# Kernel optimization log

Hardware: AMD Instinct MI355X
Metric: run time of the kernel (lower is better)

## Reference

```python
import jax, jax.numpy as jnp
import numpy as np

N, IN_CH, HID, OUT = 3072, 128, 256, 32
HEADS = 12


def setup_inputs() -> dict:
    key = jax.random.key(0)
    ks = jax.random.split(key, 16)

    def glorot(k, shape):
        fan_in, fan_out = shape[0], shape[-1]
        lim = float(np.sqrt(6.0 / (fan_in + fan_out)))
        return jax.random.uniform(k, shape, jnp.float32, -lim, lim)

    return {
        "x": jax.random.normal(ks[0], (N, IN_CH), jnp.float32),
        "attn_tensor": jax.random.normal(ks[1], (HEADS, N, N), jnp.float32),
        "edge_weight": jnp.ones((1,), jnp.float32),  # unused (use_edge_weight=False)
        "batch_idx": jnp.zeros((N,), jnp.int64),      # single graph
        # Conv2d(12,1,1) == per-head scalar mix
        "agg_w": jax.random.normal(ks[2], (HEADS,), jnp.float32) * 0.1,
        "agg_b": jnp.zeros((1,), jnp.float32),
        # GCNConv weights (x @ W then propagate, + bias)
        "W1": glorot(ks[3], (IN_CH, HID)), "b1": jnp.zeros((HID,), jnp.float32),
        "W2": glorot(ks[4], (HID, HID)),   "b2": jnp.zeros((HID,), jnp.float32),
        # final MLP: Linear -> ReLU -> LayerNorm -> Linear
        "lin1_W": glorot(ks[5], (HID, HID)), "lin1_b": jnp.zeros((HID,), jnp.float32),
        "ln_g": jnp.ones((HID,), jnp.float32), "ln_b": jnp.zeros((HID,), jnp.float32),
        "lin2_W": glorot(ks[6], (HID, OUT)), "lin2_b": jnp.zeros((OUT,), jnp.float32),
    }


def reference(x, attn_tensor, edge_weight, batch_idx,
              agg_w, agg_b, W1, b1, W2, b2,
              lin1_W, lin1_b, ln_g, ln_b, lin2_W, lin2_b):
    threshold = 0.0
    n = x.shape[0]

    # Conv2d(12,1,kernel_size=1): weighted sum over heads -> [N, N] score matrix
    agg = jnp.einsum('c,cij->ij', agg_w, attn_tensor) + agg_b[0]

    # thresholded adjacency (mask.nonzero() -> edge_index), kept dense in jax
    A = (agg > threshold).astype(x.dtype)  # A[s, t] = edge s->t

    # PyG gcn_norm with add_remaining_self_loops (binary weights -> diag = 1)
    eye = jnp.eye(n, dtype=x.dtype)
    A_hat = A * (1.0 - eye) + eye
    deg = A_hat.sum(axis=0)                        # in-degree at target nodes
    dinv = jnp.where(deg > 0, jax.lax.rsqrt(deg), 0.0)
    A_norm = dinv[:, None] * A_hat * dinv[None, :]  # norm = dinv[src] * dinv[dst]

    # GCNConv 1: out[t] = sum_s A_norm[s,t] (x W)[s] + b
    h = jnp.einsum('st,sd->td', A_norm, x @ W1) + b1
    h = jax.nn.relu(h)
    # GCNConv 2
    h = jnp.einsum('st,sd->td', A_norm, h @ W2) + b2

    # global_mean_pool over batch_idx (single graph here)
    bi = batch_idx.astype(jnp.int32)
    sums = jax.ops.segment_sum(h, bi, num_segments=1)
    counts = jax.ops.segment_sum(jnp.ones((n,), h.dtype), bi, num_segments=1)
    g = sums / counts[:, None]

    # Linear -> ReLU -> LayerNorm -> Linear
    z = jax.nn.relu(g @ lin1_W + lin1_b)
    mu = z.mean(axis=-1, keepdims=True)
    var = ((z - mu) ** 2).mean(axis=-1, keepdims=True)
    z = (z - mu) * jax.lax.rsqrt(var + 1e-5) * ln_g + ln_b
    out = z @ lin2_W + lin2_b
    return out
```

## Files before the change

### kernel.cpp

```cpp
#include <hip/hip_runtime.h>
#include <hip/hip_bf16.h>

#define NN     3072
#define NW32   96
#define INCH   128
#define HID    256
#define NHEADS 12
#define PLANE  9437184LL
#define NADJ   2304
#define CHUNK  4096

typedef __attribute__((ext_vector_type(8))) short     s16x8;
typedef __attribute__((ext_vector_type(4))) float     f32x4;
typedef __attribute__((ext_vector_type(8))) unsigned short u16x8;
typedef __attribute__((ext_vector_type(4))) unsigned int   u32x4;

__device__ inline unsigned short bf16_rne(float f) {
    unsigned int u = __float_as_uint(f);
    u += 0x7FFFu + ((u >> 16) & 1u);
    return (unsigned short)(u >> 16);
}

__global__ __launch_bounds__(256) void k_adj_y1(const float* __restrict__ attn,
                                                const float* __restrict__ agg_w,
                                                const float* __restrict__ agg_b,
                                                const float* __restrict__ x,
                                                const float* __restrict__ W1,
                                                unsigned int* __restrict__ mask32,
                                                unsigned short* __restrict__ y1t) {
    __shared__ unsigned char nib[1024];
    __shared__ float xs[8][INCH];

    if (blockIdx.x < NADJ) {
        const int b = blockIdx.x;
        const int j = threadIdx.x;
        const float thr = -agg_b[0];
        float wc[NHEADS];
#pragma unroll
        for (int c = 0; c < NHEADS; ++c) wc[c] = agg_w[c];

        f32x4 acc[4];
#pragma unroll
        for (int sl = 0; sl < 4; ++sl) acc[sl] = (f32x4){0.f, 0.f, 0.f, 0.f};

        const float* pb = attn + (long long)b * CHUNK + 4 * j;
#pragma unroll 1
        for (int c = 0; c < NHEADS; ++c) {
            const float* pc = pb + (long long)c * PLANE;
            const float w = wc[c];
            f32x4 v0 = *(const f32x4*)(pc);
            f32x4 v1 = *(const f32x4*)(pc + 1024);
            f32x4 v2 = *(const f32x4*)(pc + 2048);
            f32x4 v3 = *(const f32x4*)(pc + 3072);
#pragma unroll
            for (int k = 0; k < 4; ++k) {
                acc[0][k] = fmaf(w, v0[k], acc[0][k]);
                acc[1][k] = fmaf(w, v1[k], acc[1][k]);
                acc[2][k] = fmaf(w, v2[k], acc[2][k]);
                acc[3][k] = fmaf(w, v3[k], acc[3][k]);
            }
        }

        const unsigned B = (unsigned)b * CHUNK;
#pragma unroll
        for (int sl = 0; sl < 4; ++sl) {
            const unsigned i0 = B + sl * 1024u + 4u * j;
            unsigned bits = 0;
#pragma unroll
            for (int k = 0; k < 4; ++k) {
                bool pred = (acc[sl][k] > thr) || ((i0 + k) % 3073u == 0u);
                bits |= pred ? (1u << k) : 0u;
            }
            nib[sl * 256 + j] = (unsigned char)bits;
        }
        __syncthreads();
        if (j < 128) {
            unsigned a  = *(const unsigned*)(nib + 8 * j);
            unsigned c2 = *(const unsigned*)(nib + 8 * j + 4);
            a  &= 0x0F0F0F0Fu; a  = (a  | (a  >> 4)) & 0x00FF00FFu; a  = (a  | (a  >> 8)) & 0x0000FFFFu;
            c2 &= 0x0F0F0F0Fu; c2 = (c2 | (c2 >> 4)) & 0x00FF00FFu; c2 = (c2 | (c2 >> 8)) & 0x0000FFFFu;
            mask32[(B >> 5) + j] = a | (c2 << 16);
        }
    } else {
        int s0 = (blockIdx.x - NADJ) * 8;
        for (int i = threadIdx.x; i < 8 * INCH; i += 256)
            xs[i >> 7][i & 127] = x[s0 * INCH + i];
        __syncthreads();
        int d = threadIdx.x;
        float acc[8] = {0, 0, 0, 0, 0, 0, 0, 0};
        for (int k = 0; k < INCH; ++k) {
            float w = W1[k * HID + d];
#pragma unroll
            for (int r = 0; r < 8; ++r) acc[r] = fmaf(xs[r][k], w, acc[r]);
        }
        u16x8 v;
#pragma unroll
        for (int r = 0; r < 8; ++r) v[r] = bf16_rne(acc[r]);
        *(u16x8*)(y1t + (long long)d * NN + s0) = v;
    }
}

__global__ __launch_bounds__(256) void k_pack(const unsigned int* __restrict__ mask32,
                                              unsigned long long* __restrict__ maskT64) {
    const int w = threadIdx.x >> 6, l = threadIdx.x & 63;
    const int tile = blockIdx.x * 4 + w;
    const int sq = tile % 48, tq = tile / 48;
    const unsigned long long* m64 = (const unsigned long long*)mask32;
    unsigned long long myw = m64[(long long)(sq * 64 + l) * 48 + tq];
#pragma unroll 8
    for (int tt = 0; tt < 64; ++tt) {
        unsigned long long bal = __ballot((myw >> tt) & 1ULL);
        if (l == tt)
            maskT64[(long long)(tq * 64 + tt) * 48 + sq] = bal;
    }
}

__global__ __launch_bounds__(256) void k_dinv(const unsigned int* __restrict__ maskT32,
                                              float* __restrict__ dinv,
                                              unsigned short* __restrict__ dinvb) {
    int t = blockIdx.x * 256 + threadIdx.x;
    const u32x4* row = (const u32x4*)(maskT32 + (long long)t * NW32);
    int deg = 0;
#pragma unroll
    for (int i = 0; i < 24; ++i) {
        u32x4 v = row[i];
        deg += __popc(v[0]) + __popc(v[1]) + __popc(v[2]) + __popc(v[3]);
    }
    float di = rsqrtf((float)deg);
    dinv[t] = di;
    dinvb[t] = bf16_rne(di);
}

__global__ __launch_bounds__(256) void k_prop(const unsigned int* __restrict__ maskT32,
                                              const unsigned short* __restrict__ dinvb,
                                              const unsigned short* __restrict__ y1t,
                                              const float* __restrict__ dinv,
                                              float* __restrict__ partials,
                                              float* __restrict__ w2p) {
    if (blockIdx.x < 384) {
        const int w = threadIdx.x >> 6, l = threadIdx.x & 63;
        const int lr = l & 15, lg = l >> 4;
        const int t0 = (blockIdx.x % 48) * 64 + w * 16;
        const int d0 = ((blockIdx.x / 48) % 2) * 128;
        const int z  = blockIdx.x / 96;

        const unsigned long long* mrow =
            (const unsigned long long*)(maskT32 + (long long)(t0 + lr) * NW32) + z * 12;

        const unsigned short* B[8];
#pragma unroll
        for (int n = 0; n < 8; ++n)
            B[n] = y1t + (long long)(d0 + n * 16 + lr) * NN;

        f32x4 acc[8];
#pragma unroll
        for (int n = 0; n < 8; ++n) acc[n] = (f32x4){0.f, 0.f, 0.f, 0.f};

#pragma unroll 2
        for (int kw = 0; kw < 12; ++kw) {
            unsigned long long word = mrow[kw];
#pragma unroll
            for (int half = 0; half < 2; ++half) {
                const int k0 = z * 768 + kw * 64 + half * 32 + lg * 8;
                unsigned int bits = (unsigned int)((word >> (half * 32 + lg * 8)) & 0xFFULL);
                u16x8 dv = *(const u16x8*)(dinvb + k0);
                s16x8 av;
#pragma unroll
                for (int j = 0; j < 8; ++j)
                    av[j] = ((bits >> j) & 1u) ? (short)dv[j] : (short)0;
#pragma unroll
                for (int n = 0; n < 8; ++n) {
                    s16x8 bv = *(const s16x8*)(const void*)(B[n] + k0);
                    acc[n] = __builtin_amdgcn_mfma_f32_16x16x32_bf16(av, bv, acc[n], 0, 0, 0);
                }
            }
        }

        const int trow = t0 + lg * 4;
#pragma unroll
        for (int n = 0; n < 8; ++n) {
            const int d = d0 + n * 16 + lr;
#pragma unroll
            for (int r = 0; r < 4; ++r)
                partials[((size_t)z * NN + trow + r) * HID + d] = acc[n][r];
        }
    } else {
        __shared__ float red[4][64];
        const int r = blockIdx.x - 384;
        const int wq = r % 48;
        const int tc = r / 48;
        const int wv = threadIdx.x >> 6, l = threadIdx.x & 63;
        const unsigned long long* mt = (const unsigned long long*)maskT32;
        float acc = 0.0f;
#pragma unroll 4
        for (int it = 0; it < 64; ++it) {
            const int t = tc * 256 + wv * 64 + it;
            unsigned long long word = mt[(long long)t * 48 + wq];
            acc += ((word >> l) & 1ULL) ? dinv[t] : 0.0f;
        }
        red[wv][l] = acc;
        __syncthreads();
        if (threadIdx.x < 64)
            w2p[tc * NN + wq * 64 + threadIdx.x] =
                red[0][threadIdx.x] + red[1][threadIdx.x] + red[2][threadIdx.x] + red[3][threadIdx.x];
    }
}

__global__ __launch_bounds__(256) void k_vred(const float* __restrict__ partials,
                                              const float* __restrict__ dinv,
                                              const float* __restrict__ b1,
                                              const float* __restrict__ w2p,
                                              float* __restrict__ vp) {
    __shared__ float w2s[8];
    const int b = blockIdx.x, d = threadIdx.x;
    if (threadIdx.x < 8) {
        const int t = b * 8 + threadIdx.x;
        float a = 0.0f;
#pragma unroll
        for (int tc = 0; tc < 12; ++tc) a += w2p[tc * NN + t];
        w2s[threadIdx.x] = dinv[t] * a;
    }
    __syncthreads();
    const float bb = b1[d];
    float vacc = 0.0f;
#pragma unroll
    for (int i = 0; i < 8; ++i) {
        const int t = b * 8 + i;
        float ssum = partials[((size_t)0 * NN + t) * HID + d]
                   + partials[((size_t)1 * NN + t) * HID + d]
                   + partials[((size_t)2 * NN + t) * HID + d]
                   + partials[((size_t)3 * NN + t) * HID + d];
        float h = fmaxf(fmaf(dinv[t], ssum, bb), 0.0f);
        vacc = fmaf(w2s[i], h, vacc);
    }
    vp[b * HID + d] = vacc;
}

__global__ __launch_bounds__(256) void k_head(const float* __restrict__ vp,
                                              const float* __restrict__ W2,
                                              const float* __restrict__ b2,
                                              const float* __restrict__ l1W,
                                              const float* __restrict__ l1b,
                                              const float* __restrict__ lng,
                                              const float* __restrict__ lnb,
                                              const float* __restrict__ l2W,
                                              const float* __restrict__ l2b,
                                              float* __restrict__ out) {
    __shared__ float vs[HID], gs[HID], zs[HID], red[4];
    int d = threadIdx.x;
    float v = 0.0f;
    for (int c = 0; c < 384; ++c) v += vp[c * HID + d];
    vs[d] = v;
    __syncthreads();
    float a = 0.0f;
    for (int k = 0; k < HID; ++k) a = fmaf(vs[k], W2[k * HID + d], a);
    gs[d] = b2[d] + a * (1.0f / 3072.0f);
    __syncthreads();
    float z1 = l1b[d];
    for (int k = 0; k < HID; ++k) z1 = fmaf(gs[k], l1W[k * HID + d], z1);
    z1 = fmaxf(z1, 0.0f);
    float sum = z1;
    for (int o = 1; o < 64; o <<= 1) sum += __shfl_xor(sum, o);
    if ((d & 63) == 0) red[d >> 6] = sum;
    __syncthreads();
    float mu = (red[0] + red[1] + red[2] + red[3]) * (1.0f / 256.0f);
    __syncthreads();
    float diff = z1 - mu, sq = diff * diff;
    for (int o = 1; o < 64; o <<= 1) sq += __shfl_xor(sq, o);
    if ((d & 63) == 0) red[d >> 6] = sq;
    __syncthreads();
    float var = (red[0] + red[1] + red[2] + red[3]) * (1.0f / 256.0f);
    float zn = diff * rsqrtf(var + 1e-5f) * lng[d] + lnb[d];
    zs[d] = zn;
    __syncthreads();
    if (d < 32) {
        float o = l2b[d];
        for (int k = 0; k < HID; ++k) o = fmaf(zs[k], l2W[k * 32 + d], o);
        out[d] = o;
    }
}

extern "C" void kernel_launch(void* const* d_in, const int* in_sizes, int n_in,
                              void* d_out, int out_size, void* d_ws, size_t ws_size,
                              hipStream_t stream) {
    const float* x     = (const float*)d_in[0];
    const float* attn  = (const float*)d_in[1];
    const float* agg_w = (const float*)d_in[4];
    const float* agg_b = (const float*)d_in[5];
    const float* W1    = (const float*)d_in[6];
    const float* b1    = (const float*)d_in[7];
    const float* W2    = (const float*)d_in[8];
    const float* b2    = (const float*)d_in[9];
    const float* l1W   = (const float*)d_in[10];
    const float* l1b   = (const float*)d_in[11];
    const float* lng   = (const float*)d_in[12];
    const float* lnb   = (const float*)d_in[13];
    const float* l2W   = (const float*)d_in[14];
    const float* l2b   = (const float*)d_in[15];
    float* out = (float*)d_out;

    char* ws = (char*)d_ws;
    size_t off = 0;
    auto alloc = [&](size_t bytes) -> void* {
        off = (off + 255) & ~(size_t)255;
        void* p = ws + off;
        off += bytes;
        return p;
    };
    unsigned int*   mask32  = (unsigned int*)alloc((size_t)NN * NW32 * 4);
    unsigned int*   maskT32 = (unsigned int*)alloc((size_t)NN * NW32 * 4);
    float*          dinv  = (float*)alloc((size_t)NN * 4);
    unsigned short* dinvb = (unsigned short*)alloc((size_t)NN * 2);
    float*          w2p   = (float*)alloc((size_t)12 * NN * 4);
    unsigned short* y1t   = (unsigned short*)alloc((size_t)HID * NN * 2);
    float*          part  = (float*)alloc((size_t)4 * NN * HID * 4);
    float*          vp    = (float*)alloc((size_t)384 * HID * 4);

    hipLaunchKernelGGL(k_adj_y1, dim3(2688), dim3(256), 0, stream,
                       attn, agg_w, agg_b, x, W1, mask32, y1t);
    hipLaunchKernelGGL(k_pack,   dim3(576),  dim3(256), 0, stream,
                       mask32, (unsigned long long*)maskT32);
    hipLaunchKernelGGL(k_dinv,   dim3(12),   dim3(256), 0, stream, maskT32, dinv, dinvb);
    hipLaunchKernelGGL(k_prop,   dim3(960),  dim3(256), 0, stream,
                       maskT32, dinvb, y1t, dinv, part, w2p);
    hipLaunchKernelGGL(k_vred,   dim3(384),  dim3(256), 0, stream, part, dinv, b1, w2p, vp);
    hipLaunchKernelGGL(k_head,   dim3(1),    dim3(256), 0, stream,
                       vp, W2, b2, l1W, l1b, lng, lnb, l2W, l2b, out);
}
```

Baseline: 193.4 us.

## Fuse pipeline stages with last-block tail work and drop split-K partials

```diff
diff --git a/kernel.cpp b/kernel.cpp
--- a/kernel.cpp
+++ b/kernel.cpp
@@ -27,7 +27,8 @@
                                                 const float* __restrict__ x,
                                                 const float* __restrict__ W1,
                                                 unsigned int* __restrict__ mask32,
-                                                unsigned short* __restrict__ y1t) {
+                                                unsigned short* __restrict__ y1t,
+                                                unsigned int* __restrict__ cnt) {
     __shared__ unsigned char nib[1024];
     __shared__ float xs[8][INCH];
 
@@ -44,7 +45,7 @@
         for (int sl = 0; sl < 4; ++sl) acc[sl] = (f32x4){0.f, 0.f, 0.f, 0.f};
 
         const float* pb = attn + (long long)b * CHUNK + 4 * j;
-#pragma unroll 1
+#pragma unroll 3
         for (int c = 0; c < NHEADS; ++c) {
             const float* pc = pb + (long long)c * PLANE;
             const float w = wc[c];
@@ -82,6 +83,7 @@
             mask32[(B >> 5) + j] = a | (c2 << 16);
         }
     } else {
+        if (blockIdx.x == NADJ && threadIdx.x == 0) { cnt[0] = 0u; cnt[1] = 0u; }
         int s0 = (blockIdx.x - NADJ) * 8;
         for (int i = threadIdx.x; i < 8 * INCH; i += 256)
             xs[i >> 7][i & 127] = x[s0 * INCH + i];
@@ -100,8 +102,11 @@
     }
 }
 
-__global__ __launch_bounds__(256) void k_pack(const unsigned int* __restrict__ mask32,
-                                              unsigned long long* __restrict__ maskT64) {
+__global__ __launch_bounds__(256) void k_packDinv(const unsigned int* __restrict__ mask32,
+                                                  unsigned long long* __restrict__ maskT64,
+                                                  float* __restrict__ dinv,
+                                                  unsigned short* __restrict__ dinvb,
+                                                  unsigned int* __restrict__ cnt) {
     const int w = threadIdx.x >> 6, l = threadIdx.x & 63;
     const int tile = blockIdx.x * 4 + w;
     const int sq = tile % 48, tq = tile / 48;
@@ -113,143 +118,146 @@
         if (l == tt)
             maskT64[(long long)(tq * 64 + tt) * 48 + sq] = bal;
     }
-}
-
-__global__ __launch_bounds__(256) void k_dinv(const unsigned int* __restrict__ maskT32,
-                                              float* __restrict__ dinv,
-                                              unsigned short* __restrict__ dinvb) {
-    int t = blockIdx.x * 256 + threadIdx.x;
-    const u32x4* row = (const u32x4*)(maskT32 + (long long)t * NW32);
-    int deg = 0;
-#pragma unroll
-    for (int i = 0; i < 24; ++i) {
-        u32x4 v = row[i];
-        deg += __popc(v[0]) + __popc(v[1]) + __popc(v[2]) + __popc(v[3]);
-    }
-    float di = rsqrtf((float)deg);
-    dinv[t] = di;
-    dinvb[t] = bf16_rne(di);
-}
-
-__global__ __launch_bounds__(256) void k_prop(const unsigned int* __restrict__ maskT32,
-                                              const unsigned short* __restrict__ dinvb,
-                                              const unsigned short* __restrict__ y1t,
-                                              const float* __restrict__ dinv,
-                                              float* __restrict__ partials,
-                                              float* __restrict__ w2p) {
-    if (blockIdx.x < 384) {
-        const int w = threadIdx.x >> 6, l = threadIdx.x & 63;
-        const int lr = l & 15, lg = l >> 4;
-        const int t0 = (blockIdx.x % 48) * 64 + w * 16;
-        const int d0 = ((blockIdx.x / 48) % 2) * 128;
-        const int z  = blockIdx.x / 96;
-
-        const unsigned long long* mrow =
-            (const unsigned long long*)(maskT32 + (long long)(t0 + lr) * NW32) + z * 12;
-
-        const unsigned short* B[8];
-#pragma unroll
-        for (int n = 0; n < 8; ++n)
-            B[n] = y1t + (long long)(d0 + n * 16 + lr) * NN;
-
-        f32x4 acc[8];
-#pragma unroll
-        for (int n = 0; n < 8; ++n) acc[n] = (f32x4){0.f, 0.f, 0.f, 0.f};
+
+    __threadfence();
+    __shared__ int islast;
+    if (threadIdx.x == 0) islast = (atomicAdd(cnt, 1u) == 575u) ? 1 : 0;
+    __syncthreads();
+    if (!islast) return;
+    __threadfence();
+
+    const unsigned int* mt32 = (const unsigned int*)maskT64;
+#pragma unroll 1
+    for (int tt = 0; tt < 12; ++tt) {
+        const int t = tt * 256 + threadIdx.x;
+        const u32x4* row = (const u32x4*)(mt32 + (long long)t * NW32);
+        int deg = 0;
+#pragma unroll
+        for (int i = 0; i < 24; ++i) {
+            u32x4 v = row[i];
+            deg += __popc(v[0]) + __popc(v[1]) + __popc(v[2]) + __popc(v[3]);
+        }
+        float di = rsqrtf((float)deg);
+        dinv[t] = di;
+        dinvb[t] = bf16_rne(di);
+    }
+}
+
+__global__ __launch_bounds__(256) void k_w2sum(const unsigned int* __restrict__ mask32,
+                                               const float* __restrict__ dinv,
+                                               float* __restrict__ w2sum) {
+    const int w = threadIdx.x >> 6, l = threadIdx.x & 63;
+    const int s = blockIdx.x * 4 + w;
+    const unsigned long long* row = (const unsigned long long*)(mask32 + (size_t)s * NW32);
+    unsigned long long myword = (l < 48) ? row[l] : 0ULL;
+    float acc = 0.0f;
+#pragma unroll 8
+    for (int j = 0; j < 48; ++j) {
+        unsigned long long wj = __shfl(myword, j);
+        acc += ((wj >> l) & 1ULL) ? dinv[j * 64 + l] : 0.0f;
+    }
+#pragma unroll
+    for (int o = 1; o < 64; o <<= 1) acc += __shfl_xor(acc, o);
+    if (l == 0) w2sum[s] = dinv[s] * acc;
+}
+
+__global__ __launch_bounds__(256) void k_gemmHead(const unsigned long long* __restrict__ maskT64,
+                                                  const unsigned short* __restrict__ dinvb,
+                                                  const unsigned short* __restrict__ y1t,
+                                                  const float* __restrict__ dinv,
+                                                  const float* __restrict__ w2sum,
+                                                  const float* __restrict__ b1,
+                                                  float* __restrict__ vp,
+                                                  unsigned int* __restrict__ cnt,
+                                                  const float* __restrict__ W2,
+                                                  const float* __restrict__ b2,
+                                                  const float* __restrict__ l1W,
+                                                  const float* __restrict__ l1b,
+                                                  const float* __restrict__ lng,
+                                                  const float* __restrict__ lnb,
+                                                  const float* __restrict__ l2W,
+                                                  const float* __restrict__ l2b,
+                                                  float* __restrict__ out) {
+    __shared__ float redw[4][128];
+    const int w = threadIdx.x >> 6, l = threadIdx.x & 63;
+    const int lr = l & 15, lg = l >> 4;
+    const int tb = blockIdx.x % 48, db = blockIdx.x / 48;
+    const int t0 = tb * 64 + w * 16;
+    const int d0 = db * 128;
+
+    const unsigned long long* mrow = maskT64 + (long long)(t0 + lr) * 48;
+    const unsigned short* B[8];
+#pragma unroll
+    for (int n = 0; n < 8; ++n)
+        B[n] = y1t + (long long)(d0 + n * 16 + lr) * NN;
+
+    f32x4 acc[8];
+#pragma unroll
+    for (int n = 0; n < 8; ++n) acc[n] = (f32x4){0.f, 0.f, 0.f, 0.f};
 
 #pragma unroll 2
-        for (int kw = 0; kw < 12; ++kw) {
-            unsigned long long word = mrow[kw];
-#pragma unroll
-            for (int half = 0; half < 2; ++half) {
-                const int k0 = z * 768 + kw * 64 + half * 32 + lg * 8;
-                unsigned int bits = (unsigned int)((word >> (half * 32 + lg * 8)) & 0xFFULL);
-                u16x8 dv = *(const u16x8*)(dinvb + k0);
-                s16x8 av;
-#pragma unroll
-                for (int j = 0; j < 8; ++j)
-                    av[j] = ((bits >> j) & 1u) ? (short)dv[j] : (short)0;
-#pragma unroll
-                for (int n = 0; n < 8; ++n) {
-                    s16x8 bv = *(const s16x8*)(const void*)(B[n] + k0);
-                    acc[n] = __builtin_amdgcn_mfma_f32_16x16x32_bf16(av, bv, acc[n], 0, 0, 0);
-                }
+    for (int kw = 0; kw < 48; ++kw) {
+        unsigned long long word = mrow[kw];
+#pragma unroll
+        for (int half = 0; half < 2; ++half) {
+            const int k0 = kw * 64 + half * 32 + lg * 8;
+            unsigned int bits = (unsigned int)((word >> (half * 32 + lg * 8)) & 0xFFULL);
+            u16x8 dv = *(const u16x8*)(dinvb + k0);
+            s16x8 av;
+#pragma unroll
+            for (int j = 0; j < 8; ++j)
+                av[j] = ((bits >> j) & 1u) ? (short)dv[j] : (short)0;
+#pragma unroll
+            for (int n = 0; n < 8; ++n) {
+                s16x8 bv = *(const s16x8*)(const void*)(B[n] + k0);
+                acc[n] = __builtin_amdgcn_mfma_f32_16x16x32_bf16(av, bv, acc[n], 0, 0, 0);
             }
         }
-
-        const int trow = t0 + lg * 4;
-#pragma unroll
-        for (int n = 0; n < 8; ++n) {
-            const int d = d0 + n * 16 + lr;
-#pragma unroll
-            for (int r = 0; r < 4; ++r)
-                partials[((size_t)z * NN + trow + r) * HID + d] = acc[n][r];
-        }
-    } else {
-        __shared__ float red[4][64];
-        const int r = blockIdx.x - 384;
-        const int wq = r % 48;
-        const int tc = r / 48;
-        const int wv = threadIdx.x >> 6, l = threadIdx.x & 63;
-        const unsigned long long* mt = (const unsigned long long*)maskT32;
-        float acc = 0.0f;
+    }
+
+    float dinv_r[4], w2s_r[4];
+#pragma unroll
+    for (int r = 0; r < 4; ++r) {
+        const int t = t0 + lg * 4 + r;
+        dinv_r[r] = dinv[t];
+        w2s_r[r] = w2sum[t];
+    }
+    float p[8];
+#pragma unroll
+    for (int n = 0; n < 8; ++n) {
+        const float bb = b1[d0 + n * 16 + lr];
+        float pn = 0.0f;
+#pragma unroll
+        for (int r = 0; r < 4; ++r) {
+            float h = fmaxf(fmaf(dinv_r[r], acc[n][r], bb), 0.0f);
+            pn = fmaf(w2s_r[r], h, pn);
+        }
+        pn += __shfl_xor(pn, 16);
+        pn += __shfl_xor(pn, 32);
+        p[n] = pn;
+    }
+    if (l < 16) {
+#pragma unroll
+        for (int n = 0; n < 8; ++n) redw[w][n * 16 + l] = p[n];
+    }
+    __syncthreads();
+    if (threadIdx.x < 128)
+        vp[(size_t)blockIdx.x * 128 + threadIdx.x] =
+            redw[0][threadIdx.x] + redw[1][threadIdx.x] + redw[2][threadIdx.x] + redw[3][threadIdx.x];
+
+    __threadfence();
+    __shared__ int islast;
+    if (threadIdx.x == 0) islast = (atomicAdd(cnt + 1, 1u) == 95u) ? 1 : 0;
+    __syncthreads();
+    if (!islast) return;
+    __threadfence();
+
+    __shared__ float vs[HID], gs[HID], zs[HID], red[4];
+    const int d = threadIdx.x;
+    const int ddb = d >> 7, di = d & 127;
+    float v = 0.0f;
 #pragma unroll 4
-        for (int it = 0; it < 64; ++it) {
-            const int t = tc * 256 + wv * 64 + it;
-            unsigned long long word = mt[(long long)t * 48 + wq];
-            acc += ((word >> l) & 1ULL) ? dinv[t] : 0.0f;
-        }
-        red[wv][l] = acc;
-        __syncthreads();
-        if (threadIdx.x < 64)
-            w2p[tc * NN + wq * 64 + threadIdx.x] =
-                red[0][threadIdx.x] + red[1][threadIdx.x] + red[2][threadIdx.x] + red[3][threadIdx.x];
-    }
-}
-
-__global__ __launch_bounds__(256) void k_vred(const float* __restrict__ partials,
-                                              const float* __restrict__ dinv,
-                                              const float* __restrict__ b1,
-                                              const float* __restrict__ w2p,
-                                              float* __restrict__ vp) {
-    __shared__ float w2s[8];
-    const int b = blockIdx.x, d = threadIdx.x;
-    if (threadIdx.x < 8) {
-        const int t = b * 8 + threadIdx.x;
-        float a = 0.0f;
-#pragma unroll
-        for (int tc = 0; tc < 12; ++tc) a += w2p[tc * NN + t];
-        w2s[threadIdx.x] = dinv[t] * a;
-    }
-    __syncthreads();
-    const float bb = b1[d];
-    float vacc = 0.0f;
-#pragma unroll
-    for (int i = 0; i < 8; ++i) {
-        const int t = b * 8 + i;
-        float ssum = partials[((size_t)0 * NN + t) * HID + d]
-                   + partials[((size_t)1 * NN + t) * HID + d]
-                   + partials[((size_t)2 * NN + t) * HID + d]
-                   + partials[((size_t)3 * NN + t) * HID + d];
-        float h = fmaxf(fmaf(dinv[t], ssum, bb), 0.0f);
-        vacc = fmaf(w2s[i], h, vacc);
-    }
-    vp[b * HID + d] = vacc;
-}
-
-__global__ __launch_bounds__(256) void k_head(const float* __restrict__ vp,
-                                              const float* __restrict__ W2,
-                                              const float* __restrict__ b2,
-                                              const float* __restrict__ l1W,
-                                              const float* __restrict__ l1b,
-                                              const float* __restrict__ lng,
-                                              const float* __restrict__ lnb,
-                                              const float* __restrict__ l2W,
-                                              const float* __restrict__ l2b,
-                                              float* __restrict__ out) {
-    __shared__ float vs[HID], gs[HID], zs[HID], red[4];
-    int d = threadIdx.x;
-    float v = 0.0f;
-    for (int c = 0; c < 384; ++c) v += vp[c * HID + d];
+    for (int t = 0; t < 48; ++t) v += vp[(size_t)(ddb * 48 + t) * 128 + di];
     vs[d] = v;
     __syncthreads();
     float a = 0.0f;
@@ -311,19 +319,17 @@
     unsigned int*   maskT32 = (unsigned int*)alloc((size_t)NN * NW32 * 4);
     float*          dinv  = (float*)alloc((size_t)NN * 4);
     unsigned short* dinvb = (unsigned short*)alloc((size_t)NN * 2);
-    float*          w2p   = (float*)alloc((size_t)12 * NN * 4);
+    float*          w2sum = (float*)alloc((size_t)NN * 4);
     unsigned short* y1t   = (unsigned short*)alloc((size_t)HID * NN * 2);
-    float*          part  = (float*)alloc((size_t)4 * NN * HID * 4);
-    float*          vp    = (float*)alloc((size_t)384 * HID * 4);
-
-    hipLaunchKernelGGL(k_adj_y1, dim3(2688), dim3(256), 0, stream,
-                       attn, agg_w, agg_b, x, W1, mask32, y1t);
-    hipLaunchKernelGGL(k_pack,   dim3(576),  dim3(256), 0, stream,
-                       mask32, (unsigned long long*)maskT32);
-    hipLaunchKernelGGL(k_dinv,   dim3(12),   dim3(256), 0, stream, maskT32, dinv, dinvb);
-    hipLaunchKernelGGL(k_prop,   dim3(960),  dim3(256), 0, stream,
-                       maskT32, dinvb, y1t, dinv, part, w2p);
-    hipLaunchKernelGGL(k_vred,   dim3(384),  dim3(256), 0, stream, part, dinv, b1, w2p, vp);
-    hipLaunchKernelGGL(k_head,   dim3(1),    dim3(256), 0, stream,
-                       vp, W2, b2, l1W, l1b, lng, lnb, l2W, l2b, out);
-}
+    float*          vp    = (float*)alloc((size_t)96 * 128 * 4);
+    unsigned int*   cnt   = (unsigned int*)alloc(8);
+
+    hipLaunchKernelGGL(k_adj_y1,   dim3(2688), dim3(256), 0, stream,
+                       attn, agg_w, agg_b, x, W1, mask32, y1t, cnt);
+    hipLaunchKernelGGL(k_packDinv, dim3(576),  dim3(256), 0, stream,
+                       mask32, (unsigned long long*)maskT32, dinv, dinvb, cnt);
+    hipLaunchKernelGGL(k_w2sum,    dim3(768),  dim3(256), 0, stream, mask32, dinv, w2sum);
+    hipLaunchKernelGGL(k_gemmHead, dim3(96),   dim3(256), 0, stream,
+                       (const unsigned long long*)maskT32, dinvb, y1t, dinv, w2sum, b1,
+                       vp, cnt, W2, b2, l1W, l1b, lng, lnb, l2W, l2b, out);
+}
```

After: 410.3 us. 112% more time.
